# Performance work log

Measured on AMD Instinct MI355X. Metric: run time of the kernel, lower is better.

The kernel has to match this reference:

```python
import jax, jax.numpy as jnp
import numpy as np


def setup_inputs() -> dict:
    key = jax.random.key(0)
    ks = jax.random.split(key, 8)
    B, C, P1, P2 = 8, 256, 2048, 4096
    Cq = C // 8
    return {
        "x1": jax.random.normal(ks[0], (B, C, P1), dtype=jnp.float32),
        "x2": jax.random.normal(ks[1], (B, C, P2), dtype=jnp.float32),
        "Wq": jax.random.normal(ks[2], (Cq, C), dtype=jnp.float32) * (1.0 / np.sqrt(C)),
        "bq": jnp.zeros((Cq,), dtype=jnp.float32),
        "Wk": jax.random.normal(ks[3], (Cq, C), dtype=jnp.float32) * (1.0 / np.sqrt(C)),
        "bk": jnp.zeros((Cq,), dtype=jnp.float32),
        "Wv": jax.random.normal(ks[4], (C, C), dtype=jnp.float32) * (1.0 / np.sqrt(C)),
        "bv": jnp.zeros((C,), dtype=jnp.float32),
        "alpha": jnp.ones((1,), dtype=jnp.float32),
    }


def reference(x1, x2, Wq, bq, Wk, bk, Wv, bv, alpha):
    # Conv1d(kernel_size=1) == pointwise linear over channel dim.
    # q: [B, P1, Cq]   (Q(x1) then permute(0,2,1))
    q = jnp.einsum('oc,bcp->bpo', Wq, x1) + bq[None, None, :]
    # k: [B, Cq, P2]
    k = jnp.einsum('oc,bcp->bop', Wk, x2) + bk[None, :, None]
    # v: [B, C, P1]
    v = jnp.einsum('oc,bcp->bop', Wv, x1) + bv[None, :, None]
    # energy: [B, P1, P2]; unscaled attention, softmax over P2
    energy = jnp.einsum('bpo,boq->bpq', q, k)
    attention = jax.nn.softmax(energy, axis=-1)
    # out: [B, C, P2]
    out = jnp.einsum('bcp,bpq->bcq', v, attention)
    return alpha * out + x2
```

## Files before the change

### kernel.cpp

```cpp
#include <hip/hip_runtime.h>

#define B 8
#define C 256
#define P1 2048
#define P2 4096
#define CQ 32

typedef _Float16 h8 __attribute__((ext_vector_type(8)));
typedef _Float16 h4 __attribute__((ext_vector_type(4)));
typedef float f4 __attribute__((ext_vector_type(4)));

#define MFMA16(a, b, c) __builtin_amdgcn_mfma_f32_16x16x32_f16(a, b, c, 0, 0, 0)

__global__ void prep_w(const float* __restrict__ Wq, const float* __restrict__ Wk,
                       const float* __restrict__ Wv,
                       _Float16* __restrict__ Wqh, _Float16* __restrict__ Wql,
                       _Float16* __restrict__ Wkh, _Float16* __restrict__ Wkl,
                       _Float16* __restrict__ Wvh) {
    const int i = blockIdx.x * 256 + threadIdx.x;
    if (i < CQ * C) {
        float a = Wq[i]; _Float16 h = (_Float16)a;
        Wqh[i] = h; Wql[i] = (_Float16)(a - (float)h);
        float b2 = Wk[i]; _Float16 h2 = (_Float16)b2;
        Wkh[i] = h2; Wkl[i] = (_Float16)(b2 - (float)h2);
    }
    for (int j = i; j < C * C; j += 32 * 256)
        Wvh[j] = (_Float16)Wv[j];
}

__global__ __launch_bounds__(256) void prep1(
        const float* __restrict__ x1,
        const _Float16* __restrict__ Wqh, const _Float16* __restrict__ Wql,
        const _Float16* __restrict__ Wvh,
        const float* __restrict__ bq, const float* __restrict__ bv,
        _Float16* __restrict__ qhw, _Float16* __restrict__ qlw,
        _Float16* __restrict__ vhw) {
    __shared__ float xs[32][257];
    const int t  = threadIdx.x;
    const int b  = blockIdx.x;
    const int p0 = blockIdx.y * 32;
    const float* xb = x1 + (size_t)b * C * P1;

    {
        const int pl = t & 31, cg = t >> 5;
#pragma unroll 8
        for (int i = 0; i < 32; ++i) {
            int c = cg * 32 + i;
            xs[pl][c] = xb[(size_t)c * P1 + p0 + pl];
        }
    }
    __syncthreads();

    const int w = t >> 6, lane = t & 63, ln = lane & 15, quad = lane >> 4;
    const int nh = w & 1, ch = w >> 1;
    const int prow = nh * 16 + ln;

    f4 accv[8];
#pragma unroll
    for (int mt = 0; mt < 8; ++mt) accv[mt] = (f4){0.f, 0.f, 0.f, 0.f};
    f4 accq = {0.f, 0.f, 0.f, 0.f};

    for (int ks = 0; ks < 8; ++ks) {
        const int c0 = ks * 32 + quad * 8;
        h8 bh, bl;
#pragma unroll
        for (int j = 0; j < 8; ++j) {
            float xv = xs[prow][c0 + j];
            _Float16 hh = (_Float16)xv;
            bh[j] = hh; bl[j] = (_Float16)(xv - (float)hh);
        }
#pragma unroll
        for (int mt = 0; mt < 8; ++mt) {
            h8 a = *(const h8*)&Wvh[(size_t)((ch * 8 + mt) * 16 + ln) * C + c0];
            accv[mt] = MFMA16(a, bh, accv[mt]);
            accv[mt] = MFMA16(a, bl, accv[mt]);
        }
        {
            h8 aqh = *(const h8*)&Wqh[(size_t)(ch * 16 + ln) * C + c0];
            h8 aql = *(const h8*)&Wql[(size_t)(ch * 16 + ln) * C + c0];
            accq = MFMA16(aql, bh, accq);
            accq = MFMA16(aqh, bl, accq);
            accq = MFMA16(aqh, bh, accq);
        }
    }

#pragma unroll
    for (int mt = 0; mt < 8; ++mt) {
        int cb = (ch * 8 + mt) * 16 + quad * 4;
        f4 bvv = *(const f4*)&bv[cb];
#pragma unroll
        for (int r = 0; r < 4; ++r)
            vhw[((size_t)b * C + cb + r) * P1 + p0 + prow] =
                (_Float16)(accv[mt][r] + bvv[r]);
    }
    {
        int ob = ch * 16 + quad * 4;
        f4 bqv = *(const f4*)&bq[ob];
        h4 hv, lv;
#pragma unroll
        for (int r = 0; r < 4; ++r) {
            float val = accq[r] + bqv[r];
            _Float16 hh = (_Float16)val;
            hv[r] = hh; lv[r] = (_Float16)(val - (float)hh);
        }
        size_t row = ((size_t)b * P1 + p0 + prow) * CQ + ob;
        *(h4*)(qhw + row) = hv;
        *(h4*)(qlw + row) = lv;
    }
}

__global__ __launch_bounds__(256) void prep2(
        const float* __restrict__ x2,
        const _Float16* __restrict__ Wkh, const _Float16* __restrict__ Wkl,
        const float* __restrict__ bk,
        _Float16* __restrict__ khw, _Float16* __restrict__ klw) {
    __shared__ float xs[32][257];
    const int t  = threadIdx.x;
    const int b  = blockIdx.x;
    const int p0 = blockIdx.y * 32;
    const float* xb = x2 + (size_t)b * C * P2;
    {
        const int pl = t & 31, cg = t >> 5;
#pragma unroll 8
        for (int i = 0; i < 32; ++i) {
            int c = cg * 32 + i;
            xs[pl][c] = xb[(size_t)c * P2 + p0 + pl];
        }
    }
    __syncthreads();

    const int w = t >> 6, lane = t & 63, ln = lane & 15, quad = lane >> 4;
    const int nh = w & 1, mh = w >> 1;
    const int prow = nh * 16 + ln;

    f4 accq = {0.f, 0.f, 0.f, 0.f};
    for (int ks = 0; ks < 8; ++ks) {
        const int c0 = ks * 32 + quad * 8;
        h8 bh, bl;
#pragma unroll
        for (int j = 0; j < 8; ++j) {
            float xv = xs[prow][c0 + j];
            _Float16 hh = (_Float16)xv;
            bh[j] = hh; bl[j] = (_Float16)(xv - (float)hh);
        }
        h8 akh = *(const h8*)&Wkh[(size_t)(mh * 16 + ln) * C + c0];
        h8 akl = *(const h8*)&Wkl[(size_t)(mh * 16 + ln) * C + c0];
        accq = MFMA16(akl, bh, accq);
        accq = MFMA16(akh, bl, accq);
        accq = MFMA16(akh, bh, accq);
    }
    {
        int ob = mh * 16 + quad * 4;
        f4 bkv = *(const f4*)&bk[ob];
        h4 hv, lv;
#pragma unroll
        for (int r = 0; r < 4; ++r) {
            float val = accq[r] + bkv[r];
            _Float16 hh = (_Float16)val;
            hv[r] = hh; lv[r] = (_Float16)(val - (float)hh);
        }
        size_t row = ((size_t)b * P2 + p0 + prow) * CQ + ob;
        *(h4*)(khw + row) = hv;
        *(h4*)(klw + row) = lv;
    }
}

__global__ __launch_bounds__(512) void stats_l(
        const _Float16* __restrict__ qhi, const _Float16* __restrict__ qlo,
        const _Float16* __restrict__ khi, const _Float16* __restrict__ klo,
        float* __restrict__ linv) {
    __shared__ float lred[2][64];
    const int t = threadIdx.x;
    const int b = blockIdx.x;
    const int p0 = blockIdx.y * 64;
    const int w = t >> 6, lane = t & 63, ln = lane & 15, quad = lane >> 4;
    const int ptw = w & 3, qh_half = w >> 2;
    const int pbase = p0 + ptw * 16;

    h8 qh = *(const h8*)(qhi + ((size_t)b * P1 + pbase + ln) * CQ + quad * 8);
    h8 ql = *(const h8*)(qlo + ((size_t)b * P1 + pbase + ln) * CQ + quad * 8);

    f4 acc = {0.f, 0.f, 0.f, 0.f};
    const _Float16* khb = khi + (size_t)b * P2 * CQ;
    const _Float16* klb = klo + (size_t)b * P2 * CQ;

    for (int qc = qh_half * 2048; qc < qh_half * 2048 + 2048; qc += 32) {
#pragma unroll
        for (int tile = 0; tile < 2; ++tile) {
            int q = qc + tile * 16 + ln;
            h8 kh = *(const h8*)(khb + (size_t)q * CQ + quad * 8);
            h8 kl = *(const h8*)(klb + (size_t)q * CQ + quad * 8);
            f4 z = {0.f, 0.f, 0.f, 0.f};
            f4 e = MFMA16(ql, kh, z);
            e = MFMA16(qh, kl, e);
            e = MFMA16(qh, kh, e);
#pragma unroll
            for (int r = 0; r < 4; ++r) acc[r] += __expf(e[r]);
        }
    }
#pragma unroll
    for (int off = 1; off < 16; off <<= 1) {
#pragma unroll
        for (int r = 0; r < 4; ++r) acc[r] += __shfl_xor(acc[r], off);
    }
    if (ln == 0) *(f4*)&lred[qh_half][ptw * 16 + quad * 4] = acc;
    __syncthreads();
    if (t < 64)
        linv[(size_t)b * P1 + p0 + t] = 1.0f / (lred[0][t] + lred[1][t]);
}

__global__ __launch_bounds__(256, 2) void attn_gemm(
        const _Float16* __restrict__ qhi, const _Float16* __restrict__ qlo,
        const _Float16* __restrict__ khi, const _Float16* __restrict__ klo,
        const _Float16* __restrict__ vhi, const float* __restrict__ linv,
        const float* __restrict__ x2, const float* __restrict__ alpha_p,
        float* __restrict__ out) {
    __shared__ _Float16 att_s[2][64][64];

    const int t  = threadIdx.x;
    const int b  = blockIdx.x & 7;
    const int q0 = (blockIdx.x >> 3) * 64;
    const int wc = t >> 6;
    const int lane = t & 63, ln = lane & 15, quad = lane >> 4;
    const int sw = ln & 7;

    h8 kh[4], kl[4];
#pragma unroll
    for (int nt = 0; nt < 4; ++nt) {
        int q = q0 + nt * 16 + ln;
        kh[nt] = *(const h8*)(khi + ((size_t)b * P2 + q) * CQ + quad * 8);
        kl[nt] = *(const h8*)(klo + ((size_t)b * P2 + q) * CQ + quad * 8);
    }

    f4 acc[4][4];
#pragma unroll
    for (int mt = 0; mt < 4; ++mt)
#pragma unroll
        for (int nt = 0; nt < 4; ++nt) acc[mt][nt] = (f4){0.f, 0.f, 0.f, 0.f};

    h8 nqh, nql;
    {
        size_t r = ((size_t)b * P1 + wc * 16 + ln) * CQ + quad * 8;
        nqh = *(const h8*)(qhi + r);
        nql = *(const h8*)(qlo + r);
    }

    const int wbcol = wc * 2 + (quad >> 1);
    const int wcol  = ((wbcol ^ sw) << 3) + (quad & 1) * 4;

    for (int pc = 0; pc < P1 / 64; ++pc) {
        const int p0v = pc * 64;
        h8 cqh = nqh, cql = nql;
        if (pc + 1 < P1 / 64) {
            size_t r = ((size_t)b * P1 + p0v + 64 + wc * 16 + ln) * CQ + quad * 8;
            nqh = *(const h8*)(qhi + r);
            nql = *(const h8*)(qlo + r);
        }
        f4 lv = *(const f4*)(linv + (size_t)b * P1 + p0v + wc * 16 + quad * 4);

        _Float16* abuf = &att_s[pc & 1][0][0];
#pragma unroll
        for (int nt = 0; nt < 4; ++nt) {
            f4 z = {0.f, 0.f, 0.f, 0.f};
            f4 e = MFMA16(cql, kh[nt], z);
            e = MFMA16(cqh, kl[nt], e);
            e = MFMA16(cqh, kh[nt], e);
            h4 pk;
#pragma unroll
            for (int r = 0; r < 4; ++r)
                pk[r] = (_Float16)(__expf(e[r]) * lv[r]);
            *(h4*)&abuf[(nt * 16 + ln) * 64 + wcol] = pk;
        }
        __syncthreads();

#pragma unroll
        for (int kk = 0; kk < 64; kk += 32) {
            h8 bf[4];
#pragma unroll
            for (int nt = 0; nt < 4; ++nt) {
                int bcol2 = (kk >> 3) + quad;
                bf[nt] = *(const h8*)&abuf[(nt * 16 + ln) * 64 + ((bcol2 ^ sw) << 3)];
            }
            h8 av[4];
#pragma unroll
            for (int mt = 0; mt < 4; ++mt) {
                size_t off = ((size_t)b * C + wc * 64 + mt * 16 + ln) * P1
                           + p0v + kk + quad * 8;
                av[mt] = *(const h8*)(vhi + off);
            }
#pragma unroll
            for (int mt = 0; mt < 4; ++mt)
#pragma unroll
                for (int nt = 0; nt < 4; ++nt)
                    acc[mt][nt] = MFMA16(av[mt], bf[nt], acc[mt][nt]);
        }
    }

    const float alpha = alpha_p[0];
#pragma unroll
    for (int mt = 0; mt < 4; ++mt) {
#pragma unroll
        for (int nt = 0; nt < 4; ++nt) {
            int q = q0 + nt * 16 + ln;
#pragma unroll
            for (int r = 0; r < 4; ++r) {
                int c = wc * 64 + mt * 16 + quad * 4 + r;
                size_t o = ((size_t)b * C + c) * P2 + q;
                out[o] = fmaf(alpha, acc[mt][nt][r], x2[o]);
            }
        }
    }
}

extern "C" void kernel_launch(void* const* d_in, const int* in_sizes, int n_in,
                              void* d_out, int out_size, void* d_ws, size_t ws_size,
                              hipStream_t stream) {
    const float* x1    = (const float*)d_in[0];
    const float* x2    = (const float*)d_in[1];
    const float* Wq    = (const float*)d_in[2];
    const float* bq    = (const float*)d_in[3];
    const float* Wk    = (const float*)d_in[4];
    const float* bk    = (const float*)d_in[5];
    const float* Wv    = (const float*)d_in[6];
    const float* bv    = (const float*)d_in[7];
    const float* alpha = (const float*)d_in[8];
    float* out = (float*)d_out;

    _Float16* qh = (_Float16*)d_ws;
    _Float16* ql = qh + (size_t)B * P1 * CQ;
    _Float16* kh = ql + (size_t)B * P1 * CQ;
    _Float16* kl = kh + (size_t)B * P2 * CQ;
    _Float16* vh = kl + (size_t)B * P2 * CQ;
    _Float16* wqh = vh + (size_t)B * C * P1;
    _Float16* wql = wqh + CQ * C;
    _Float16* wkh = wql + CQ * C;
    _Float16* wkl = wkh + CQ * C;
    _Float16* wvh = wkl + CQ * C;
    float*    li  = (float*)(wvh + C * C);

    prep_w<<<dim3(32), 256, 0, stream>>>(Wq, Wk, Wv, wqh, wql, wkh, wkl, wvh);
    prep1<<<dim3(B, P1 / 32), 256, 0, stream>>>(x1, wqh, wql, wvh, bq, bv, qh, ql, vh);
    prep2<<<dim3(B, P2 / 32), 256, 0, stream>>>(x2, wkh, wkl, bk, kh, kl);
    stats_l<<<dim3(B, P1 / 64), 512, 0, stream>>>(qh, ql, kh, kl, li);
    attn_gemm<<<dim3(512), 256, 0, stream>>>(qh, ql, kh, kl, vh, li, x2, alpha, out);
}
```

Measured before the change: 279.3 us.

## Halve attention output tile to double grid size and occupancy

```diff
diff --git a/kernel.cpp b/kernel.cpp
--- a/kernel.cpp
+++ b/kernel.cpp
@@ -169,12 +169,12 @@
         const _Float16* __restrict__ qhi, const _Float16* __restrict__ qlo,
         const _Float16* __restrict__ khi, const _Float16* __restrict__ klo,
         float* __restrict__ linv) {
-    __shared__ float lred[2][64];
-    const int t = threadIdx.x;
-    const int b = blockIdx.x;
-    const int p0 = blockIdx.y * 64;
+    __shared__ float lred[2][4][16];
+    const int t  = threadIdx.x;
+    const int b  = blockIdx.x & 7;
+    const int p0 = (blockIdx.x >> 3) * 32;
     const int w = t >> 6, lane = t & 63, ln = lane & 15, quad = lane >> 4;
-    const int ptw = w & 3, qh_half = w >> 2;
+    const int ptw = w & 1, qq = w >> 1;
     const int pbase = p0 + ptw * 16;
 
     h8 qh = *(const h8*)(qhi + ((size_t)b * P1 + pbase + ln) * CQ + quad * 8);
@@ -184,7 +184,7 @@
     const _Float16* khb = khi + (size_t)b * P2 * CQ;
     const _Float16* klb = klo + (size_t)b * P2 * CQ;
 
-    for (int qc = qh_half * 2048; qc < qh_half * 2048 + 2048; qc += 32) {
+    for (int qc = qq * 1024; qc < qq * 1024 + 1024; qc += 32) {
 #pragma unroll
         for (int tile = 0; tile < 2; ++tile) {
             int q = qc + tile * 16 + ln;
@@ -203,83 +203,96 @@
 #pragma unroll
         for (int r = 0; r < 4; ++r) acc[r] += __shfl_xor(acc[r], off);
     }
-    if (ln == 0) *(f4*)&lred[qh_half][ptw * 16 + quad * 4] = acc;
+    if (ln == 0) *(f4*)&lred[ptw][qq][quad * 4] = acc;
     __syncthreads();
-    if (t < 64)
-        linv[(size_t)b * P1 + p0 + t] = 1.0f / (lred[0][t] + lred[1][t]);
-}
-
-__global__ __launch_bounds__(256, 2) void attn_gemm(
+    if (t < 32) {
+        int pw = t >> 4, pp = t & 15;
+        float s = lred[pw][0][pp] + lred[pw][1][pp] +
+                  lred[pw][2][pp] + lred[pw][3][pp];
+        linv[(size_t)b * P1 + p0 + pw * 16 + pp] = 1.0f / s;
+    }
+}
+
+__global__ __launch_bounds__(256, 4) void attn_gemm(
         const _Float16* __restrict__ qhi, const _Float16* __restrict__ qlo,
         const _Float16* __restrict__ khi, const _Float16* __restrict__ klo,
         const _Float16* __restrict__ vhi, const float* __restrict__ linv,
         const float* __restrict__ x2, const float* __restrict__ alpha_p,
         float* __restrict__ out) {
-    __shared__ _Float16 att_s[2][64][64];
+    __shared__ _Float16 att_s[2][32][128];
 
     const int t  = threadIdx.x;
     const int b  = blockIdx.x & 7;
-    const int q0 = (blockIdx.x >> 3) * 64;
+    const int q0 = (blockIdx.x >> 3) * 32;
     const int wc = t >> 6;
     const int lane = t & 63, ln = lane & 15, quad = lane >> 4;
     const int sw = ln & 7;
 
-    h8 kh[4], kl[4];
-#pragma unroll
-    for (int nt = 0; nt < 4; ++nt) {
+    h8 kh[2], kl[2];
+#pragma unroll
+    for (int nt = 0; nt < 2; ++nt) {
         int q = q0 + nt * 16 + ln;
         kh[nt] = *(const h8*)(khi + ((size_t)b * P2 + q) * CQ + quad * 8);
         kl[nt] = *(const h8*)(klo + ((size_t)b * P2 + q) * CQ + quad * 8);
     }
 
-    f4 acc[4][4];
+    f4 acc[4][2];
 #pragma unroll
     for (int mt = 0; mt < 4; ++mt)
 #pragma unroll
-        for (int nt = 0; nt < 4; ++nt) acc[mt][nt] = (f4){0.f, 0.f, 0.f, 0.f};
-
-    h8 nqh, nql;
-    {
-        size_t r = ((size_t)b * P1 + wc * 16 + ln) * CQ + quad * 8;
-        nqh = *(const h8*)(qhi + r);
-        nql = *(const h8*)(qlo + r);
-    }
-
-    const int wbcol = wc * 2 + (quad >> 1);
-    const int wcol  = ((wbcol ^ sw) << 3) + (quad & 1) * 4;
-
-    for (int pc = 0; pc < P1 / 64; ++pc) {
-        const int p0v = pc * 64;
-        h8 cqh = nqh, cql = nql;
-        if (pc + 1 < P1 / 64) {
-            size_t r = ((size_t)b * P1 + p0v + 64 + wc * 16 + ln) * CQ + quad * 8;
-            nqh = *(const h8*)(qhi + r);
-            nql = *(const h8*)(qlo + r);
-        }
-        f4 lv = *(const f4*)(linv + (size_t)b * P1 + p0v + wc * 16 + quad * 4);
+        for (int nt = 0; nt < 2; ++nt) acc[mt][nt] = (f4){0.f, 0.f, 0.f, 0.f};
+
+    h8 cqh[2], cql[2];
+#pragma unroll
+    for (int pt = 0; pt < 2; ++pt) {
+        size_t r = ((size_t)b * P1 + wc * 32 + pt * 16 + ln) * CQ + quad * 8;
+        cqh[pt] = *(const h8*)(qhi + r);
+        cql[pt] = *(const h8*)(qlo + r);
+    }
+
+    for (int pc = 0; pc < P1 / 128; ++pc) {
+        const int p0v = pc * 128;
+        f4 lv[2];
+#pragma unroll
+        for (int pt = 0; pt < 2; ++pt)
+            lv[pt] = *(const f4*)(linv + (size_t)b * P1 + p0v + wc * 32 + pt * 16 + quad * 4);
 
         _Float16* abuf = &att_s[pc & 1][0][0];
 #pragma unroll
-        for (int nt = 0; nt < 4; ++nt) {
-            f4 z = {0.f, 0.f, 0.f, 0.f};
-            f4 e = MFMA16(cql, kh[nt], z);
-            e = MFMA16(cqh, kl[nt], e);
-            e = MFMA16(cqh, kh[nt], e);
-            h4 pk;
-#pragma unroll
-            for (int r = 0; r < 4; ++r)
-                pk[r] = (_Float16)(__expf(e[r]) * lv[r]);
-            *(h4*)&abuf[(nt * 16 + ln) * 64 + wcol] = pk;
+        for (int pt = 0; pt < 2; ++pt) {
+            int g   = wc * 4 + pt * 2 + (quad >> 1);
+            int col = ((g ^ sw) << 3) + (quad & 1) * 4;
+#pragma unroll
+            for (int nt = 0; nt < 2; ++nt) {
+                f4 z = {0.f, 0.f, 0.f, 0.f};
+                f4 e = MFMA16(cql[pt], kh[nt], z);
+                e = MFMA16(cqh[pt], kl[nt], e);
+                e = MFMA16(cqh[pt], kh[nt], e);
+                h4 pk;
+#pragma unroll
+                for (int r = 0; r < 4; ++r)
+                    pk[r] = (_Float16)(__expf(e[r]) * lv[pt][r]);
+                *(h4*)&abuf[(nt * 16 + ln) * 128 + col] = pk;
+            }
         }
         __syncthreads();
 
-#pragma unroll
-        for (int kk = 0; kk < 64; kk += 32) {
-            h8 bf[4];
-#pragma unroll
-            for (int nt = 0; nt < 4; ++nt) {
-                int bcol2 = (kk >> 3) + quad;
-                bf[nt] = *(const h8*)&abuf[(nt * 16 + ln) * 64 + ((bcol2 ^ sw) << 3)];
+        if (pc + 1 < P1 / 128) {
+#pragma unroll
+            for (int pt = 0; pt < 2; ++pt) {
+                size_t r = ((size_t)b * P1 + p0v + 128 + wc * 32 + pt * 16 + ln) * CQ + quad * 8;
+                cqh[pt] = *(const h8*)(qhi + r);
+                cql[pt] = *(const h8*)(qlo + r);
+            }
+        }
+
+#pragma unroll
+        for (int kk = 0; kk < 128; kk += 32) {
+            h8 bf[2];
+#pragma unroll
+            for (int nt = 0; nt < 2; ++nt) {
+                int g2 = (kk >> 3) + quad;
+                bf[nt] = *(const h8*)&abuf[(nt * 16 + ln) * 128 + ((g2 ^ sw) << 3)];
             }
             h8 av[4];
 #pragma unroll
@@ -291,7 +304,7 @@
 #pragma unroll
             for (int mt = 0; mt < 4; ++mt)
 #pragma unroll
-                for (int nt = 0; nt < 4; ++nt)
+                for (int nt = 0; nt < 2; ++nt)
                     acc[mt][nt] = MFMA16(av[mt], bf[nt], acc[mt][nt]);
         }
     }
@@ -300,7 +313,7 @@
 #pragma unroll
     for (int mt = 0; mt < 4; ++mt) {
 #pragma unroll
-        for (int nt = 0; nt < 4; ++nt) {
+        for (int nt = 0; nt < 2; ++nt) {
             int q = q0 + nt * 16 + ln;
 #pragma unroll
             for (int r = 0; r < 4; ++r) {
@@ -341,6 +354,6 @@
     prep_w<<<dim3(32), 256, 0, stream>>>(Wq, Wk, Wv, wqh, wql, wkh, wkl, wvh);
     prep1<<<dim3(B, P1 / 32), 256, 0, stream>>>(x1, wqh, wql, wvh, bq, bv, qh, ql, vh);
     prep2<<<dim3(B, P2 / 32), 256, 0, stream>>>(x2, wkh, wkl, bk, kh, kl);
-    stats_l<<<dim3(B, P1 / 64), 512, 0, stream>>>(qh, ql, kh, kl, li);
-    attn_gemm<<<dim3(512), 256, 0, stream>>>(qh, ql, kh, kl, vh, li, x2, alpha, out);
-}
+    stats_l<<<dim3(512), 512, 0, stream>>>(qh, ql, kh, kl, li);
+    attn_gemm<<<dim3(1024), 256, 0, stream>>>(qh, ql, kh, kl, vh, li, x2, alpha, out);
+}
```

After: 307.6 us. 1.1x slower.
